# Kernel optimization log

Hardware: AMD Instinct MI355X
Metric: run time of the kernel (lower is better)

Reference implementation:

```python
import jax, jax.numpy as jnp
import numpy as np
from jax import lax

NEG_SLOPE = 0.2
BN_EPS = 1e-5


def _edges(n_nodes, n_total):
    # complete graph (no self loops) on the first n_nodes nodes, as in create_complete_graph,
    # plus PyG GATConv default add_self_loops over ALL n_total nodes.
    i = np.arange(n_nodes)
    src = np.repeat(i, n_nodes)
    dst = np.tile(i, n_nodes)
    keep = src != dst
    loops = np.arange(n_total)
    src = np.concatenate([src[keep], loops]).astype(np.int32)
    dst = np.concatenate([dst[keep], loops]).astype(np.int32)
    return jnp.asarray(src), jnp.asarray(dst)


def _bn_eval(x, g, b, m, v):
    # x: [B, C, H, W]; eval-mode batchnorm with running stats
    inv = g / jnp.sqrt(v + BN_EPS)
    return x * inv[None, :, None, None] + (b - m * inv)[None, :, None, None]


def _gat(x, W, a_src, a_dst, bias, src, dst, n_total):
    h = x @ W                      # [N, D_out]
    s = h @ a_src                  # [N] per-node source score
    d = h @ a_dst                  # [N] per-node dest score
    e = jax.nn.leaky_relu(s[src] + d[dst], NEG_SLOPE)          # [E]
    emax = jax.ops.segment_max(e, dst, num_segments=n_total)   # [N]
    ex = jnp.exp(e - emax[dst])
    denom = jax.ops.segment_sum(ex, dst, num_segments=n_total)
    alpha = ex / denom[dst]                                    # [E]
    out = jax.ops.segment_sum(alpha[:, None] * h[src], dst, num_segments=n_total)
    return out + bias


def setup_inputs() -> dict:
    key = jax.random.key(0)
    ks = jax.random.split(key, 12)
    B, H, W = 8, 64, 64

    def rn(k, shape, s):
        return jax.random.normal(k, shape, jnp.float32) * s

    return {
        "images": jax.random.normal(ks[0], (B, 3, H, W), jnp.float32),
        "conv1_w": rn(ks[1], (64, 3, 3, 3), 0.1), "conv1_b": jnp.zeros((64,), jnp.float32),
        "bn1_g": jnp.ones((64,), jnp.float32), "bn1_b": jnp.zeros((64,), jnp.float32),
        "bn1_m": jnp.zeros((64,), jnp.float32), "bn1_v": jnp.ones((64,), jnp.float32),
        "conv2_w": rn(ks[2], (128, 64, 3, 3), 0.05), "conv2_b": jnp.zeros((128,), jnp.float32),
        "bn2_g": jnp.ones((128,), jnp.float32), "bn2_b": jnp.zeros((128,), jnp.float32),
        "bn2_m": jnp.zeros((128,), jnp.float32), "bn2_v": jnp.ones((128,), jnp.float32),
        "gat1_w": rn(ks[3], (128, 256), 0.05), "gat1_asrc": rn(ks[4], (256,), 0.05),
        "gat1_adst": rn(ks[5], (256,), 0.05), "gat1_bias": jnp.zeros((256,), jnp.float32),
        "gat2_w": rn(ks[6], (256, 128), 0.05), "gat2_asrc": rn(ks[7], (128,), 0.05),
        "gat2_adst": rn(ks[8], (128,), 0.05), "gat2_bias": jnp.zeros((128,), jnp.float32),
        "out_w": rn(ks[9], (128, 10), 0.05), "out_b": jnp.zeros((10,), jnp.float32),
    }


def reference(images, conv1_w, conv1_b, bn1_g, bn1_b, bn1_m, bn1_v,
              conv2_w, conv2_b, bn2_g, bn2_b, bn2_m, bn2_v,
              gat1_w, gat1_asrc, gat1_adst, gat1_bias,
              gat2_w, gat2_asrc, gat2_adst, gat2_bias,
              out_w, out_b):
    dn = ("NCHW", "OIHW", "NCHW")
    x = lax.conv_general_dilated(images, conv1_w, (1, 1), "SAME", dimension_numbers=dn)
    x = x + conv1_b[None, :, None, None]
    x = jax.nn.relu(_bn_eval(x, bn1_g, bn1_b, bn1_m, bn1_v))
    x = lax.reduce_window(x, -jnp.inf, lax.max, (1, 1, 2, 2), (1, 1, 2, 2), "VALID")
    x = lax.conv_general_dilated(x, conv2_w, (1, 1), "SAME", dimension_numbers=dn)
    x = x + conv2_b[None, :, None, None]
    x = jax.nn.relu(_bn_eval(x, bn2_g, bn2_b, bn2_m, bn2_v))

    B = x.shape[0]
    n_nodes = x.shape[2] * x.shape[3]          # (H/2)*(W/2) = 1024
    x = x.reshape(B, 128, n_nodes).transpose(0, 2, 1).reshape(-1, 128)  # [B*n, 128]
    n_total = B * n_nodes
    src, dst = _edges(n_nodes, n_total)

    x = jax.nn.relu(_gat(x, gat1_w, gat1_asrc, gat1_adst, gat1_bias, src, dst, n_total))
    x = jax.nn.relu(_gat(x, gat2_w, gat2_asrc, gat2_adst, gat2_bias, src, dst, n_total))

    x = x.reshape(B, n_nodes, 128).mean(axis=1)   # global_mean_pool over each image's nodes
    logits = x @ out_w + out_b
    return jax.nn.log_softmax(logits, axis=1)
```

## Files before the change

### kernel.cpp

```cpp
#include <hip/hip_runtime.h>
#include <math.h>

#define BN_EPS 1e-5f
#define NEG_SLOPE 0.2f

__device__ __forceinline__ float relu_f(float x) { return x > 0.f ? x : 0.f; }
__device__ __forceinline__ float leaky_f(float z) { return z > 0.f ? z : NEG_SLOPE * z; }

__global__ void conv1_pool(const float* __restrict__ img, const float* __restrict__ w,
                           const float* __restrict__ cb, const float* __restrict__ g,
                           const float* __restrict__ bb, const float* __restrict__ m,
                           const float* __restrict__ vv, float* __restrict__ out)
{
    int blk = blockIdx.x;
    int q = blk & 3, cog = (blk >> 2) & 15, b = blk >> 6;
    int t = threadIdx.x;
    int x = t & 31, y = (q << 3) + (t >> 5);

    float acc[4][4] = {};
#pragma unroll
    for (int ci = 0; ci < 3; ++ci) {
        const float* ib = img + (b * 3 + ci) * 4096;
        float rv[4][4];
#pragma unroll
        for (int r = 0; r < 4; ++r) {
            int yy = 2 * y - 1 + r;
            bool yok = (unsigned)yy < 64u;
            const float* p = ib + yy * 64 + 2 * x;
            float2 c01 = yok ? *(const float2*)p : make_float2(0.f, 0.f);
            rv[r][1] = c01.x;
            rv[r][2] = c01.y;
            rv[r][0] = (yok && x > 0) ? p[-1] : 0.f;
            rv[r][3] = (yok && x < 31) ? p[2] : 0.f;
        }
#pragma unroll
        for (int j = 0; j < 4; ++j) {
            const float* wj = w + ((cog * 4 + j) * 3 + ci) * 9;
#pragma unroll
            for (int ky = 0; ky < 3; ++ky)
#pragma unroll
                for (int kx = 0; kx < 3; ++kx) {
                    float wvv = wj[ky * 3 + kx];
#pragma unroll
                    for (int py = 0; py < 2; ++py)
#pragma unroll
                        for (int px = 0; px < 2; ++px)
                            acc[j][py * 2 + px] += rv[py + ky][px + kx] * wvv;
                }
        }
    }
#pragma unroll
    for (int j = 0; j < 4; ++j) {
        int co = cog * 4 + j;
        float inv = g[co] / sqrtf(vv[co] + BN_EPS);
        float sh = cb[co] * inv + (bb[co] - m[co] * inv);
        float v0 = relu_f(acc[j][0] * inv + sh);
        float v1 = relu_f(acc[j][1] * inv + sh);
        float v2 = relu_f(acc[j][2] * inv + sh);
        float v3 = relu_f(acc[j][3] * inv + sh);
        out[((b * 64 + co) * 32 + y) * 32 + x] = fmaxf(fmaxf(v0, v1), fmaxf(v2, v3));
    }
}

__global__ void conv2_split(const float* __restrict__ in, const float* __restrict__ w,
                            float* __restrict__ pacc01, float* __restrict__ pacc23)
{
    int blk = blockIdx.x;
    int kz = blk & 3, half = (blk >> 2) & 1, cog = (blk >> 3) & 31, b = blk >> 8;
    int t = threadIdx.x;
    int x2p = (t & 15) * 2;
    int y = half * 16 + (t >> 4);
    bool xnz = x2p != 0;
    bool xhi = x2p == 30;
    const float* ibase = in + b * 64 * 1024 + kz * 16 * 1024;
    int xb = xnz ? x2p - 1 : 0;

    float acc[4][2] = {};

#pragma unroll 2
    for (int ci = 0; ci < 16; ++ci) {
        const float* cb2 = ibase + ci * 1024;
        float rc[3][4];
#pragma unroll
        for (int r = 0; r < 3; ++r) {
            int yy = y - 1 + r;
            bool yok = (unsigned)yy < 32u;
            const float* p = cb2 + yy * 32 + xb;
            float4 f = yok ? *(const float4*)p : make_float4(0.f, 0.f, 0.f, 0.f);
            rc[r][0] = xnz ? f.x : 0.f;
            rc[r][1] = xnz ? f.y : f.x;
            rc[r][2] = xnz ? f.z : f.y;
            float r3 = xnz ? f.w : f.z;
            rc[r][3] = xhi ? 0.f : r3;
        }
#pragma unroll
        for (int j = 0; j < 4; ++j) {
            const float* wj = w + ((cog * 4 + j) * 64 + kz * 16 + ci) * 9;
#pragma unroll
            for (int ky = 0; ky < 3; ++ky)
#pragma unroll
                for (int kx = 0; kx < 3; ++kx) {
                    float wvv = wj[ky * 3 + kx];
                    acc[j][0] += rc[ky][kx] * wvv;
                    acc[j][1] += rc[ky][kx + 1] * wvv;
                }
        }
    }

    int n0 = b * 1024 + y * 32 + x2p;
    float* pp = (kz & 2 ? pacc23 : pacc01) + (size_t)(kz & 1) * 1048576;
    float4 s0 = {acc[0][0], acc[1][0], acc[2][0], acc[3][0]};
    float4 s1 = {acc[0][1], acc[1][1], acc[2][1], acc[3][1]};
    *(float4*)&pp[(size_t)n0 * 128 + cog * 4] = s0;
    *(float4*)&pp[(size_t)(n0 + 1) * 128 + cog * 4] = s1;
}

__global__ void conv2_combine(const float* __restrict__ pacc01, const float* __restrict__ pacc23,
                              const float* __restrict__ cb, const float* __restrict__ g,
                              const float* __restrict__ bb, const float* __restrict__ m,
                              const float* __restrict__ vv, float* __restrict__ x0)
{
    int idx = blockIdx.x * blockDim.x + threadIdx.x;
    int c4 = idx & 31;
    const float4* p01 = (const float4*)pacc01;
    const float4* p23 = (const float4*)pacc23;
    float4 a0 = p01[idx];
    float4 a1 = p01[idx + 262144];
    float4 a2 = p23[idx];
    float4 a3 = p23[idx + 262144];
    float sx = a0.x + a1.x + a2.x + a3.x;
    float sy = a0.y + a1.y + a2.y + a3.y;
    float sz = a0.z + a1.z + a2.z + a3.z;
    float sw = a0.w + a1.w + a2.w + a3.w;

    float4 gg = ((const float4*)g)[c4];
    float4 vvv = ((const float4*)vv)[c4];
    float4 bbb = ((const float4*)bb)[c4];
    float4 mm = ((const float4*)m)[c4];
    float4 cbb = ((const float4*)cb)[c4];
    float ix = gg.x / sqrtf(vvv.x + BN_EPS);
    float iy = gg.y / sqrtf(vvv.y + BN_EPS);
    float iz = gg.z / sqrtf(vvv.z + BN_EPS);
    float iw = gg.w / sqrtf(vvv.w + BN_EPS);
    float shx = cbb.x * ix + (bbb.x - mm.x * ix);
    float shy = cbb.y * iy + (bbb.y - mm.y * iy);
    float shz = cbb.z * iz + (bbb.z - mm.z * iz);
    float shw = cbb.w * iw + (bbb.w - mm.w * iw);

    float4 o = {relu_f(sx * ix + shx), relu_f(sy * iy + shy),
                relu_f(sz * iz + shz), relu_f(sw * iw + shw)};
    ((float4*)x0)[idx] = o;
}

template <int K, int N>
__global__ void gemm32(const float* __restrict__ A, const float* __restrict__ B,
                       float* __restrict__ C)
{
    __shared__ float As[16][32];
    __shared__ float Bs[16][64];
    int t = threadIdx.x;
    int m0 = blockIdx.x * 32;
    int n0 = blockIdx.y * 64;
    int tx = t & 15, ty = t >> 4;
    int am = t >> 2, akq = (t & 3) * 4;
    float acc[4][4] = {};

    for (int k0 = 0; k0 < K; k0 += 16) {
        float4 av = *(const float4*)&A[(size_t)(m0 + am) * K + k0 + akq];
        float4 bv0 = *(const float4*)&B[(size_t)(k0 + ty) * N + n0 + tx * 4];
        float4 bv1 = *(const float4*)&B[(size_t)(k0 + 8 + ty) * N + n0 + tx * 4];
        __syncthreads();
        As[akq + 0][am] = av.x;
        As[akq + 1][am] = av.y;
        As[akq + 2][am] = av.z;
        As[akq + 3][am] = av.w;
        *(float4*)&Bs[ty][tx * 4] = bv0;
        *(float4*)&Bs[ty + 8][tx * 4] = bv1;
        __syncthreads();
#pragma unroll
        for (int kk = 0; kk < 16; ++kk) {
            float4 a4 = *(const float4*)&As[kk][ty * 4];
            float4 b4 = *(const float4*)&Bs[kk][tx * 4];
            float aa[4] = {a4.x, a4.y, a4.z, a4.w};
            float bb4[4] = {b4.x, b4.y, b4.z, b4.w};
#pragma unroll
            for (int i = 0; i < 4; ++i)
#pragma unroll
                for (int j = 0; j < 4; ++j)
                    acc[i][j] += aa[i] * bb4[j];
        }
    }
#pragma unroll
    for (int i = 0; i < 4; ++i) {
        float4 o = {acc[i][0], acc[i][1], acc[i][2], acc[i][3]};
        *(float4*)&C[(size_t)(m0 + ty * 4 + i) * N + n0 + tx * 4] = o;
    }
}

__global__ void score_kernel(const float* __restrict__ h, const float* __restrict__ asrc,
                             const float* __restrict__ adst, float* __restrict__ s,
                             float* __restrict__ d, int D, int N)
{
    int gt = blockIdx.x * blockDim.x + threadIdx.x;
    int wave = gt >> 6, lane = gt & 63;
    if (wave >= N) return;
    const float* hp = h + (size_t)wave * D;
    float ss = 0.f, dd = 0.f;
    for (int c = lane; c < D; c += 64) {
        float hv = hp[c];
        ss += hv * asrc[c];
        dd += hv * adst[c];
    }
    for (int off = 32; off; off >>= 1) {
        ss += __shfl_down(ss, off);
        dd += __shfl_down(dd, off);
    }
    if (lane == 0) { s[wave] = ss; d[wave] = dd; }
}

template <int D, int KS>
__global__ void gat_agg_gemm(const float* __restrict__ h, const float* __restrict__ s,
                             const float* __restrict__ d, float* __restrict__ pacc,
                             float* __restrict__ pden)
{
    __shared__ float Ss[1024];
    __shared__ float As[16][32];
    __shared__ float Bs[16][64];
    __shared__ float red[2];
    __shared__ float part[16][32];

    const int CH = 1024 / KS;
    int t = threadIdx.x;
    int m0 = blockIdx.x * 32;
    int n0 = blockIdx.y * 64;
    int kz = blockIdx.z;
    int tx = t & 15, ty = t >> 4;
    int ug = t >> 3, vg4 = (t & 7) * 4;

    float4 sa = *(const float4*)&s[t * 8];
    float4 sb = *(const float4*)&s[t * 8 + 4];
    *(float4*)&Ss[t * 8] = sa;
    *(float4*)&Ss[t * 8 + 4] = sb;
    float lm = fmaxf(fmaxf(fmaxf(sa.x, sa.y), fmaxf(sa.z, sa.w)),
                     fmaxf(fmaxf(sb.x, sb.y), fmaxf(sb.z, sb.w)));
#pragma unroll
    for (int off = 1; off < 64; off <<= 1) lm = fmaxf(lm, __shfl_xor(lm, off));
    if ((t & 63) == 0) red[t >> 6] = lm;
    __syncthreads();
    float smax = fmaxf(red[0], red[1]);

    float4 dv = *(const float4*)&d[m0 + vg4];
    float4 mv = {leaky_f(smax + dv.x), leaky_f(smax + dv.y),
                 leaky_f(smax + dv.z), leaky_f(smax + dv.w)};
    float4 dsum = {0.f, 0.f, 0.f, 0.f};
    float acc[4][4] = {};

    for (int k0 = kz * CH; k0 < kz * CH + CH; k0 += 16) {
        float4 bv0 = *(const float4*)&h[(size_t)(k0 + ty) * D + n0 + tx * 4];
        float4 bv1 = *(const float4*)&h[(size_t)(k0 + 8 + ty) * D + n0 + tx * 4];
        float su = Ss[k0 + ug];
        float4 avv;
        avv.x = __expf(leaky_f(su + dv.x) - mv.x);
        avv.y = __expf(leaky_f(su + dv.y) - mv.y);
        avv.z = __expf(leaky_f(su + dv.z) - mv.z);
        avv.w = __expf(leaky_f(su + dv.w) - mv.w);
        dsum.x += avv.x; dsum.y += avv.y; dsum.z += avv.z; dsum.w += avv.w;
        __syncthreads();
        *(float4*)&As[ug][vg4] = avv;
        *(float4*)&Bs[ty][tx * 4] = bv0;
        *(float4*)&Bs[ty + 8][tx * 4] = bv1;
        __syncthreads();
#pragma unroll
        for (int kk = 0; kk < 16; ++kk) {
            float4 a4 = *(const float4*)&As[kk][ty * 4];
            float4 b4 = *(const float4*)&Bs[kk][tx * 4];
            float aa[4] = {a4.x, a4.y, a4.z, a4.w};
            float bb4[4] = {b4.x, b4.y, b4.z, b4.w};
#pragma unroll
            for (int i = 0; i < 4; ++i)
#pragma unroll
                for (int j = 0; j < 4; ++j)
                    acc[i][j] += aa[i] * bb4[j];
        }
    }

    __syncthreads();
    *(float4*)&part[ug][vg4] = dsum;
    __syncthreads();

#pragma unroll
    for (int i = 0; i < 4; ++i) {
        int r = ty * 4 + i;
        float4 o = {acc[i][0], acc[i][1], acc[i][2], acc[i][3]};
        *(float4*)&pacc[((size_t)kz * 1024 + m0 + r) * D + n0 + tx * 4] = o;
    }
    if (t < 32) {
        float den = 0.f;
#pragma unroll
        for (int u = 0; u < 16; ++u) den += part[u][t];
        pden[kz * 1024 + m0 + t] = den;
    }
}

template <int D, int KS>
__global__ void gat_combine(const float* __restrict__ pacc, const float* __restrict__ pden,
                            const float* __restrict__ bias, float* __restrict__ out)
{
    int idx = blockIdx.x * blockDim.x + threadIdx.x;
    if (idx >= 1024 * D / 4) return;
    int c4 = idx & (D / 4 - 1);
    int v = idx / (D / 4);
    float4 a = {0.f, 0.f, 0.f, 0.f};
    float den = 0.f;
#pragma unroll
    for (int ks = 0; ks < KS; ++ks) {
        float4 p = ((const float4*)pacc)[(size_t)(ks * 1024 + v) * (D / 4) + c4];
        a.x += p.x; a.y += p.y; a.z += p.z; a.w += p.w;
        den += pden[ks * 1024 + v];
    }
    float rd = 1.f / den;
    float4 bz = ((const float4*)bias)[c4];
    float4 o = {relu_f(a.x * rd + bz.x), relu_f(a.y * rd + bz.y),
                relu_f(a.z * rd + bz.z), relu_f(a.w * rd + bz.w)};
    ((float4*)out)[(size_t)v * (D / 4) + c4] = o;
}

template <int D>
__global__ void gat_self4(const float* __restrict__ h, const float* __restrict__ bias,
                          float* __restrict__ out)
{
    int idx = blockIdx.x * blockDim.x + threadIdx.x;
    if (idx >= 7168 * D / 4) return;
    int c4 = idx & (D / 4 - 1);
    int n = 1024 + idx / (D / 4);
    float4 v = ((const float4*)h)[(size_t)n * (D / 4) + c4];
    float4 bz = ((const float4*)bias)[c4];
    float4 o = {relu_f(v.x + bz.x), relu_f(v.y + bz.y),
                relu_f(v.z + bz.z), relu_f(v.w + bz.w)};
    ((float4*)out)[(size_t)n * (D / 4) + c4] = o;
}

__global__ void pool_part(const float* __restrict__ x2, float* __restrict__ part)
{
    int b = blockIdx.x >> 4, seg = blockIdx.x & 15, t = threadIdx.x;
    const float* p = x2 + ((size_t)b * 1024 + seg * 64) * 128 + t;
    float acc = 0.f;
#pragma unroll 8
    for (int n = 0; n < 64; ++n) acc += p[(size_t)n * 128];
    part[(b * 16 + seg) * 128 + t] = acc;
}

__global__ void head_kernel(const float* __restrict__ part, const float* __restrict__ ow,
                            const float* __restrict__ ob, float* __restrict__ out)
{
    __shared__ float pooled[128];
    __shared__ float logits[10];
    int b = blockIdx.x, t = threadIdx.x;
    float acc = 0.f;
#pragma unroll
    for (int sgi = 0; sgi < 16; ++sgi) acc += part[(b * 16 + sgi) * 128 + t];
    pooled[t] = acc * (1.f / 1024.f);
    __syncthreads();
    if (t < 10) {
        float l = ob[t];
        for (int c = 0; c < 128; ++c) l += pooled[c] * ow[c * 10 + t];
        logits[t] = l;
    }
    __syncthreads();
    if (t == 0) {
        float mx = logits[0];
        for (int j = 1; j < 10; ++j) mx = fmaxf(mx, logits[j]);
        float sum = 0.f;
        for (int j = 0; j < 10; ++j) sum += expf(logits[j] - mx);
        float lse = mx + logf(sum);
        for (int j = 0; j < 10; ++j) out[b * 10 + j] = logits[j] - lse;
    }
}

extern "C" void kernel_launch(void* const* d_in, const int* in_sizes, int n_in,
                              void* d_out, int out_size, void* d_ws, size_t ws_size,
                              hipStream_t stream)
{
    const float* images = (const float*)d_in[0];
    const float* c1w = (const float*)d_in[1];
    const float* c1b = (const float*)d_in[2];
    const float* bn1g = (const float*)d_in[3];
    const float* bn1b = (const float*)d_in[4];
    const float* bn1m = (const float*)d_in[5];
    const float* bn1v = (const float*)d_in[6];
    const float* c2w = (const float*)d_in[7];
    const float* c2b = (const float*)d_in[8];
    const float* bn2g = (const float*)d_in[9];
    const float* bn2b = (const float*)d_in[10];
    const float* bn2m = (const float*)d_in[11];
    const float* bn2v = (const float*)d_in[12];
    const float* g1w = (const float*)d_in[13];
    const float* g1as = (const float*)d_in[14];
    const float* g1ad = (const float*)d_in[15];
    const float* g1b = (const float*)d_in[16];
    const float* g2w = (const float*)d_in[17];
    const float* g2as = (const float*)d_in[18];
    const float* g2ad = (const float*)d_in[19];
    const float* g2b = (const float*)d_in[20];
    const float* ow = (const float*)d_in[21];
    const float* ob = (const float*)d_in[22];
    float* out = (float*)d_out;

    float* ws = (float*)d_ws;
    float* x1    = ws;
    float* bufc1 = ws + 2097152;
    float* h1    = ws + 2621440;
    float* x0    = ws + 4718592;
    float* h2    = ws + 5767168;
    float* s1    = ws + 6815744;
    float* d1    = ws + 6816768;
    float* s2    = ws + 6817792;
    float* d2    = ws + 6818816;
    float* part  = bufc1;
    float* pden1 = bufc1 + 16384;
    float* pden2 = bufc1 + 24576;
    float* pacc1 = x0;
    float* pacc2 = h1;
    float* x2    = x0;
    float* c2p01 = x1;
    float* c2p23 = h1;

    conv1_pool<<<512, 256, 0, stream>>>(images, c1w, c1b, bn1g, bn1b, bn1m, bn1v, bufc1);
    conv2_split<<<2048, 256, 0, stream>>>(bufc1, c2w, c2p01, c2p23);
    conv2_combine<<<1024, 256, 0, stream>>>(c2p01, c2p23, c2b, bn2g, bn2b, bn2m, bn2v, x0);

    gemm32<128, 256><<<dim3(256, 4), 128, 0, stream>>>(x0, g1w, h1);
    score_kernel<<<256, 256, 0, stream>>>(h1, g1as, g1ad, s1, d1, 256, 1024);
    gat_agg_gemm<256, 8><<<dim3(32, 4, 8), 128, 0, stream>>>(h1, s1, d1, pacc1, pden1);
    gat_combine<256, 8><<<256, 256, 0, stream>>>(pacc1, pden1, g1b, x1);
    gat_self4<256><<<1792, 256, 0, stream>>>(h1, g1b, x1);

    gemm32<256, 128><<<dim3(256, 2), 128, 0, stream>>>(x1, g2w, h2);
    score_kernel<<<256, 256, 0, stream>>>(h2, g2as, g2ad, s2, d2, 128, 1024);
    gat_agg_gemm<128, 16><<<dim3(32, 2, 16), 128, 0, stream>>>(h2, s2, d2, pacc2, pden2);
    gat_combine<128, 16><<<128, 256, 0, stream>>>(pacc2, pden2, g2b, x2);
    gat_self4<128><<<896, 256, 0, stream>>>(h2, g2b, x2);

    pool_part<<<128, 128, 0, stream>>>(x2, part);
    head_kernel<<<8, 128, 0, stream>>>(part, ow, ob, out);
}
```

Before: 215.2 us.

## Fuse self-loop bias+relu into consumers and merge pool with head

Drops the gat_self4 kernels. Nodes 1024 and above, which only have self loops, now get their bias+ReLU applied inside the next GEMM's A-load, or inside a fused pool+head kernel that reads h2 directly. Conv2 partial sums are stored in a contiguous per-thread layout, so the combine kernel reads them coalesced and scatters to NHWC itself. This saves launches and a full write plus reread of the self-loop activations. In exchange it adds a branch in the GEMM, and the pool now runs on only 8 blocks, which reduces parallelism.

```diff
diff --git a/kernel.cpp b/kernel.cpp
--- a/kernel.cpp
+++ b/kernel.cpp
@@ -107,37 +107,44 @@
         }
     }
 
-    int n0 = b * 1024 + y * 32 + x2p;
     float* pp = (kz & 2 ? pacc23 : pacc01) + (size_t)(kz & 1) * 1048576;
+    int bid = b * 64 + cog * 2 + half;
+    size_t base = ((size_t)bid * 256 + t) * 8;
     float4 s0 = {acc[0][0], acc[1][0], acc[2][0], acc[3][0]};
     float4 s1 = {acc[0][1], acc[1][1], acc[2][1], acc[3][1]};
-    *(float4*)&pp[(size_t)n0 * 128 + cog * 4] = s0;
-    *(float4*)&pp[(size_t)(n0 + 1) * 128 + cog * 4] = s1;
-}
-
-__global__ void conv2_combine(const float* __restrict__ pacc01, const float* __restrict__ pacc23,
+    *(float4*)&pp[base] = s0;
+    *(float4*)&pp[base + 4] = s1;
+}
+
+__global__ void conv2_combine(const float* __restrict__ p01, const float* __restrict__ p23,
                               const float* __restrict__ cb, const float* __restrict__ g,
                               const float* __restrict__ bb, const float* __restrict__ m,
                               const float* __restrict__ vv, float* __restrict__ x0)
 {
-    int idx = blockIdx.x * blockDim.x + threadIdx.x;
-    int c4 = idx & 31;
-    const float4* p01 = (const float4*)pacc01;
-    const float4* p23 = (const float4*)pacc23;
-    float4 a0 = p01[idx];
-    float4 a1 = p01[idx + 262144];
-    float4 a2 = p23[idx];
-    float4 a3 = p23[idx + 262144];
-    float sx = a0.x + a1.x + a2.x + a3.x;
-    float sy = a0.y + a1.y + a2.y + a3.y;
-    float sz = a0.z + a1.z + a2.z + a3.z;
-    float sw = a0.w + a1.w + a2.w + a3.w;
-
-    float4 gg = ((const float4*)g)[c4];
-    float4 vvv = ((const float4*)vv)[c4];
-    float4 bbb = ((const float4*)bb)[c4];
-    float4 mm = ((const float4*)m)[c4];
-    float4 cbb = ((const float4*)cb)[c4];
+    int gid = blockIdx.x * 256 + threadIdx.x;
+    int t = gid & 255, bid = gid >> 8;
+    int half = bid & 1, cog = (bid >> 1) & 31, b = bid >> 6;
+    size_t off = (size_t)gid * 8;
+
+    float4 s0 = {0.f, 0.f, 0.f, 0.f}, s1 = {0.f, 0.f, 0.f, 0.f};
+    const float* pl0 = p01;
+    const float* pl1 = p01 + 1048576;
+    const float* pl2 = p23;
+    const float* pl3 = p23 + 1048576;
+#pragma unroll
+    for (int kz = 0; kz < 4; ++kz) {
+        const float* pp = kz == 0 ? pl0 : kz == 1 ? pl1 : kz == 2 ? pl2 : pl3;
+        float4 u0 = *(const float4*)&pp[off];
+        float4 u1 = *(const float4*)&pp[off + 4];
+        s0.x += u0.x; s0.y += u0.y; s0.z += u0.z; s0.w += u0.w;
+        s1.x += u1.x; s1.y += u1.y; s1.z += u1.z; s1.w += u1.w;
+    }
+
+    float4 gg = ((const float4*)g)[cog];
+    float4 vvv = ((const float4*)vv)[cog];
+    float4 bbb = ((const float4*)bb)[cog];
+    float4 mm = ((const float4*)m)[cog];
+    float4 cbb = ((const float4*)cb)[cog];
     float ix = gg.x / sqrtf(vvv.x + BN_EPS);
     float iy = gg.y / sqrtf(vvv.y + BN_EPS);
     float iz = gg.z / sqrtf(vvv.z + BN_EPS);
@@ -147,14 +154,21 @@
     float shz = cbb.z * iz + (bbb.z - mm.z * iz);
     float shw = cbb.w * iw + (bbb.w - mm.w * iw);
 
-    float4 o = {relu_f(sx * ix + shx), relu_f(sy * iy + shy),
-                relu_f(sz * iz + shz), relu_f(sw * iw + shw)};
-    ((float4*)x0)[idx] = o;
-}
-
-template <int K, int N>
-__global__ void gemm32(const float* __restrict__ A, const float* __restrict__ B,
-                       float* __restrict__ C)
+    float4 o0 = {relu_f(s0.x * ix + shx), relu_f(s0.y * iy + shy),
+                 relu_f(s0.z * iz + shz), relu_f(s0.w * iw + shw)};
+    float4 o1 = {relu_f(s1.x * ix + shx), relu_f(s1.y * iy + shy),
+                 relu_f(s1.z * iz + shz), relu_f(s1.w * iw + shw)};
+
+    int y = half * 16 + (t >> 4), x2p = (t & 15) * 2;
+    int n0 = b * 1024 + y * 32 + x2p;
+    *(float4*)&x0[(size_t)n0 * 128 + cog * 4] = o0;
+    *(float4*)&x0[(size_t)(n0 + 1) * 128 + cog * 4] = o1;
+}
+
+template <int K, int N, bool SELF>
+__global__ void gemm32(const float* __restrict__ A, const float* __restrict__ Ahi,
+                       const float* __restrict__ abias,
+                       const float* __restrict__ B, float* __restrict__ C)
 {
     __shared__ float As[16][32];
     __shared__ float Bs[16][64];
@@ -163,10 +177,19 @@
     int n0 = blockIdx.y * 64;
     int tx = t & 15, ty = t >> 4;
     int am = t >> 2, akq = (t & 3) * 4;
+    bool hi = SELF && m0 >= 1024;
+    const float* Ab = hi ? Ahi : A;
     float acc[4][4] = {};
 
     for (int k0 = 0; k0 < K; k0 += 16) {
-        float4 av = *(const float4*)&A[(size_t)(m0 + am) * K + k0 + akq];
+        float4 av = *(const float4*)&Ab[(size_t)(m0 + am) * K + k0 + akq];
+        if (hi) {
+            float4 bz = *(const float4*)&abias[k0 + akq];
+            av.x = relu_f(av.x + bz.x);
+            av.y = relu_f(av.y + bz.y);
+            av.z = relu_f(av.z + bz.z);
+            av.w = relu_f(av.w + bz.w);
+        }
         float4 bv0 = *(const float4*)&B[(size_t)(k0 + ty) * N + n0 + tx * 4];
         float4 bv1 = *(const float4*)&B[(size_t)(k0 + 8 + ty) * N + n0 + tx * 4];
         __syncthreads();
@@ -325,45 +348,43 @@
     ((float4*)out)[(size_t)v * (D / 4) + c4] = o;
 }
 
-template <int D>
-__global__ void gat_self4(const float* __restrict__ h, const float* __restrict__ bias,
-                          float* __restrict__ out)
-{
-    int idx = blockIdx.x * blockDim.x + threadIdx.x;
-    if (idx >= 7168 * D / 4) return;
-    int c4 = idx & (D / 4 - 1);
-    int n = 1024 + idx / (D / 4);
-    float4 v = ((const float4*)h)[(size_t)n * (D / 4) + c4];
-    float4 bz = ((const float4*)bias)[c4];
-    float4 o = {relu_f(v.x + bz.x), relu_f(v.y + bz.y),
-                relu_f(v.z + bz.z), relu_f(v.w + bz.w)};
-    ((float4*)out)[(size_t)n * (D / 4) + c4] = o;
-}
-
-__global__ void pool_part(const float* __restrict__ x2, float* __restrict__ part)
-{
-    int b = blockIdx.x >> 4, seg = blockIdx.x & 15, t = threadIdx.x;
-    const float* p = x2 + ((size_t)b * 1024 + seg * 64) * 128 + t;
-    float acc = 0.f;
-#pragma unroll 8
-    for (int n = 0; n < 64; ++n) acc += p[(size_t)n * 128];
-    part[(b * 16 + seg) * 128 + t] = acc;
-}
-
-__global__ void head_kernel(const float* __restrict__ part, const float* __restrict__ ow,
-                            const float* __restrict__ ob, float* __restrict__ out)
-{
+__global__ void poolhead(const float* __restrict__ x2low, const float* __restrict__ h2,
+                         const float* __restrict__ bias2, const float* __restrict__ ow,
+                         const float* __restrict__ ob, float* __restrict__ out)
+{
+    __shared__ float red[256];
     __shared__ float pooled[128];
     __shared__ float logits[10];
     int b = blockIdx.x, t = threadIdx.x;
-    float acc = 0.f;
-#pragma unroll
-    for (int sgi = 0; sgi < 16; ++sgi) acc += part[(b * 16 + sgi) * 128 + t];
-    pooled[t] = acc * (1.f / 1024.f);
+    int c = t & 127, hseg = t >> 7;
+    float a0 = 0.f, a1 = 0.f, a2 = 0.f, a3 = 0.f;
+    if (b == 0) {
+        const float* p = x2low + ((size_t)hseg * 512) * 128 + c;
+#pragma unroll 2
+        for (int n = 0; n < 512; n += 4) {
+            a0 += p[(size_t)n * 128];
+            a1 += p[(size_t)(n + 1) * 128];
+            a2 += p[(size_t)(n + 2) * 128];
+            a3 += p[(size_t)(n + 3) * 128];
+        }
+    } else {
+        float bz = bias2[c];
+        const float* p = h2 + ((size_t)b * 1024 + hseg * 512) * 128 + c;
+#pragma unroll 2
+        for (int n = 0; n < 512; n += 4) {
+            a0 += relu_f(p[(size_t)n * 128] + bz);
+            a1 += relu_f(p[(size_t)(n + 1) * 128] + bz);
+            a2 += relu_f(p[(size_t)(n + 2) * 128] + bz);
+            a3 += relu_f(p[(size_t)(n + 3) * 128] + bz);
+        }
+    }
+    red[t] = (a0 + a1) + (a2 + a3);
+    __syncthreads();
+    if (t < 128) pooled[t] = (red[t] + red[t + 128]) * (1.f / 1024.f);
     __syncthreads();
     if (t < 10) {
         float l = ob[t];
-        for (int c = 0; c < 128; ++c) l += pooled[c] * ow[c * 10 + t];
+        for (int cc = 0; cc < 128; ++cc) l += pooled[cc] * ow[cc * 10 + t];
         logits[t] = l;
     }
     __syncthreads();
@@ -416,7 +437,6 @@
     float* d1    = ws + 6816768;
     float* s2    = ws + 6817792;
     float* d2    = ws + 6818816;
-    float* part  = bufc1;
     float* pden1 = bufc1 + 16384;
     float* pden2 = bufc1 + 24576;
     float* pacc1 = x0;
@@ -427,20 +447,17 @@
 
     conv1_pool<<<512, 256, 0, stream>>>(images, c1w, c1b, bn1g, bn1b, bn1m, bn1v, bufc1);
     conv2_split<<<2048, 256, 0, stream>>>(bufc1, c2w, c2p01, c2p23);
-    conv2_combine<<<1024, 256, 0, stream>>>(c2p01, c2p23, c2b, bn2g, bn2b, bn2m, bn2v, x0);
-
-    gemm32<128, 256><<<dim3(256, 4), 128, 0, stream>>>(x0, g1w, h1);
+    conv2_combine<<<512, 256, 0, stream>>>(c2p01, c2p23, c2b, bn2g, bn2b, bn2m, bn2v, x0);
+
+    gemm32<128, 256, false><<<dim3(256, 4), 128, 0, stream>>>(x0, x0, nullptr, g1w, h1);
     score_kernel<<<256, 256, 0, stream>>>(h1, g1as, g1ad, s1, d1, 256, 1024);
     gat_agg_gemm<256, 8><<<dim3(32, 4, 8), 128, 0, stream>>>(h1, s1, d1, pacc1, pden1);
     gat_combine<256, 8><<<256, 256, 0, stream>>>(pacc1, pden1, g1b, x1);
-    gat_self4<256><<<1792, 256, 0, stream>>>(h1, g1b, x1);
-
-    gemm32<256, 128><<<dim3(256, 2), 128, 0, stream>>>(x1, g2w, h2);
+
+    gemm32<256, 128, true><<<dim3(256, 2), 128, 0, stream>>>(x1, h1, g1b, g2w, h2);
     score_kernel<<<256, 256, 0, stream>>>(h2, g2as, g2ad, s2, d2, 128, 1024);
     gat_agg_gemm<128, 16><<<dim3(32, 2, 16), 128, 0, stream>>>(h2, s2, d2, pacc2, pden2);
     gat_combine<128, 16><<<128, 256, 0, stream>>>(pacc2, pden2, g2b, x2);
-    gat_self4<128><<<896, 256, 0, stream>>>(h2, g2b, x2);
-
-    pool_part<<<128, 128, 0, stream>>>(x2, part);
-    head_kernel<<<8, 128, 0, stream>>>(part, ow, ob, out);
-}
+
+    poolhead<<<8, 256, 0, stream>>>(x2, h2, g2b, ow, ob, out);
+}
```

Result: slower. 227.1 us (+5.5%).
